# Performance work log

Hardware: AMD Instinct MI355X
Metric: run time of the kernel (lower is better)

The kernel has to match this reference:

```python
import jax, jax.numpy as jnp
import numpy as np

N = 50000        # nodes
E = 800000       # edges
E_PAIR = 200000  # pos/neg link pairs
IN = 256
HID = (512, 256, 160)
NEG_SLOPE = 0.2


def _lin_w(k, i, o):
    s = 1.0 / np.sqrt(i)
    return jax.random.uniform(k, (i, o), jnp.float32, -s, s)


def setup_inputs() -> dict:
    key = jax.random.key(0)
    ks = jax.random.split(key, 16)
    inp = {
        'x': jax.random.normal(ks[0], (N, IN), jnp.float32),
        'w': jax.random.uniform(ks[1], (E,), jnp.float32),
        'src': jax.random.randint(ks[2], (E,), 0, N),
        'dst': jax.random.randint(ks[3], (E,), 0, N),
        'pos_src': jax.random.randint(ks[4], (E_PAIR,), 0, N),
        'pos_dst': jax.random.randint(ks[5], (E_PAIR,), 0, N),
        'neg_src': jax.random.randint(ks[6], (E_PAIR,), 0, N),
        'neg_dst': jax.random.randint(ks[7], (E_PAIR,), 0, N),
        # GraphConv weights/biases
        'W1': _lin_w(ks[8], IN, HID[0]), 'b1': jnp.zeros((HID[0],), jnp.float32),
        'W2': _lin_w(ks[9], HID[0], HID[1]), 'b2': jnp.zeros((HID[1],), jnp.float32),
        'W3': _lin_w(ks[10], HID[1], HID[2]), 'b3': jnp.zeros((HID[2],), jnp.float32),
        # predictor MLP: 160 -> 80 -> 40 -> 1
        'P1': _lin_w(ks[11], HID[2], HID[2] // 2), 'pb1': jnp.zeros((HID[2] // 2,), jnp.float32),
        'P2': _lin_w(ks[12], HID[2] // 2, HID[2] // 4), 'pb2': jnp.zeros((HID[2] // 4,), jnp.float32),
        'P3': _lin_w(ks[13], HID[2] // 4, 1), 'pb3': jnp.zeros((1,), jnp.float32),
    }
    return inp


def _degree_norms(src, dst):
    ones = jnp.ones((E,), jnp.float32)
    out_deg = jnp.clip(jax.ops.segment_sum(ones, src, num_segments=N), 1.0)
    in_deg = jnp.clip(jax.ops.segment_sum(ones, dst, num_segments=N), 1.0)
    # norm='both': D_out^{-1/2} on source side, D_in^{-1/2} on dest side
    return (out_deg ** -0.5)[:, None], (in_deg ** -0.5)[:, None]


def _graph_conv(h, W, b, src, dst, w, out_norm, in_norm, project_first):
    # DGL GraphConv (norm='both', edge_weight=w): scale src feats, multiply
    # messages by edge weight, sum-aggregate, scale by in-degree norm, + bias.
    # DGL projects before aggregation iff in_feats > out_feats (same math).
    h = h * out_norm
    if project_first:
        h = h @ W
    agg = jax.ops.segment_sum(h[src] * w[:, None], dst, num_segments=N)
    if not project_first:
        agg = agg @ W
    return agg * in_norm + b


def _predictor(z, P1, pb1, P2, pb2, P3, pb3):
    z = jax.nn.leaky_relu(z @ P1 + pb1, NEG_SLOPE)
    z = jax.nn.leaky_relu(z @ P2 + pb2, NEG_SLOPE)
    return z @ P3 + pb3


def reference(x, w, src, dst, pos_src, pos_dst, neg_src, neg_dst,
              W1, b1, W2, b2, W3, b3, P1, pb1, P2, pb2, P3, pb3):
    out_norm, in_norm = _degree_norms(src, dst)
    h = _graph_conv(x, W1, b1, src, dst, w, out_norm, in_norm, project_first=False)  # 256<=512
    h = jax.nn.relu(h)
    h = _graph_conv(h, W2, b2, src, dst, w, out_norm, in_norm, project_first=True)   # 512>256
    h = jax.nn.relu(h)
    h = _graph_conv(h, W3, b3, src, dst, w, out_norm, in_norm, project_first=True)   # 256>160
    h_pos = _predictor(h[pos_src] * h[pos_dst], P1, pb1, P2, pb2, P3, pb3)
    h_neg = _predictor(h[neg_src] * h[neg_dst], P1, pb1, P2, pb2, P3, pb3)
    return h_pos, h_neg, h
```

## Files before the change

### kernel.cpp

```cpp
#include <hip/hip_runtime.h>
#include <math.h>

#define NN 50000
#define EE 800000
#define NPAIR 200000

typedef unsigned short u16;
typedef short short8v __attribute__((ext_vector_type(8)));
typedef float float16v __attribute__((ext_vector_type(16)));

__device__ __forceinline__ float leaky(float x){ return x >= 0.f ? x : 0.2f*x; }

__device__ __forceinline__ u16 bfhi(float x){
  union{float f; unsigned u;} v; v.f = x;
  unsigned r = (v.u + 0x7FFFu + ((v.u >> 16) & 1u)) >> 16;
  return (u16)r;
}
__device__ __forceinline__ float bf2f(u16 h){
  union{unsigned u; float f;} v; v.u = ((unsigned)h) << 16; return v.f;
}
__device__ __forceinline__ void split2(float x, float y, unsigned &hp, unsigned &lp){
  u16 hx = bfhi(x), hy = bfhi(y);
  u16 lx = bfhi(x - bf2f(hx)), ly = bfhi(y - bf2f(hy));
  hp = (unsigned)hx | ((unsigned)hy << 16);
  lp = (unsigned)lx | ((unsigned)ly << 16);
}
#define MFMA_BF16 __builtin_amdgcn_mfma_f32_32x32x16_bf16


__global__ void degree_kernel(const int* __restrict__ src, const int* __restrict__ dst,
                              int* cnt_out, int* cnt_in){
  int i = blockIdx.x*blockDim.x + threadIdx.x;
  if(i < EE){
    atomicAdd(&cnt_out[src[i]], 1);
    atomicAdd(&cnt_in[dst[i]], 1);
  }
}

__global__ void norm_kernel(const int* __restrict__ cnt_out, const int* __restrict__ cnt_in,
                            float* __restrict__ out_norm, float* __restrict__ in_norm){
  int i = blockIdx.x*blockDim.x + threadIdx.x;
  if(i < NN){
    int o = cnt_out[i]; if(o < 1) o = 1;
    int d = cnt_in[i];  if(d < 1) d = 1;
    out_norm[i] = 1.f/sqrtf((float)o);
    in_norm[i]  = 1.f/sqrtf((float)d);
  }
}

__global__ void scan_kernel(const int* __restrict__ cnt, int* __restrict__ row_off){
  const int T = 512;
  __shared__ int sums[T];
  int t = threadIdx.x;
  int chunk = (NN + T - 1)/T;
  int base = t*chunk;
  int hi = base + chunk; if(hi > NN) hi = NN;
  int s = 0;
  for(int i = base; i < hi; i++) s += cnt[i];
  sums[t] = s;
  __syncthreads();
  for(int off = 1; off < T; off <<= 1){
    int add = (t >= off) ? sums[t-off] : 0;
    __syncthreads();
    sums[t] += add;
    __syncthreads();
  }
  int run = sums[t] - s;
  for(int i = base; i < hi; i++){ row_off[i] = run; run += cnt[i]; }
  if(t == T-1) row_off[NN] = EE;
}

__global__ void bucket_kernel(const int* __restrict__ src, const int* __restrict__ dst,
                              const float* __restrict__ w, const float* __restrict__ out_norm,
                              const int* __restrict__ row_off,
                              int* fill, int* __restrict__ es, float* __restrict__ ew){
  int i = blockIdx.x*blockDim.x + threadIdx.x;
  if(i < EE){
    int d = dst[i];
    int s = src[i];
    int p = row_off[d] + atomicAdd(&fill[d], 1);
    es[p] = s;
    ew[p] = w[i] * out_norm[s];
  }
}

__global__ void wsplit_kernel(const float* __restrict__ W, int K, int M,
                              u16* __restrict__ Whi, u16* __restrict__ Wlo){
  int i = blockIdx.x*256 + threadIdx.x;
  if(i < K*M){
    int m = i / K, k = i - m*K;
    float a = W[(size_t)k*M + m];
    u16 h = bfhi(a);
    Whi[i] = h;
    Wlo[i] = bfhi(a - bf2f(h));
  }
}

__global__ void psplit_kernel(const float* __restrict__ P1, const float* __restrict__ P2,
                              u16* __restrict__ P1th, u16* __restrict__ P1tl,
                              u16* __restrict__ P2th, u16* __restrict__ P2tl){
  int i = blockIdx.x*256 + threadIdx.x;
  if(i < 96*160){
    int c = i/160, k = i - c*160;
    float v = (c < 80) ? P1[k*80 + c] : 0.f;
    u16 h = bfhi(v);
    P1th[i] = h; P1tl[i] = bfhi(v - bf2f(h));
  }
  if(i < 64*80){
    int c = i/80, k = i - c*80;
    float v = (c < 40) ? P2[k*40 + c] : 0.f;
    u16 h = bfhi(v);
    P2th[i] = h; P2tl[i] = bfhi(v - bf2f(h));
  }
}

template<int F, int MODE>
__global__ __launch_bounds__(256) void agg_kernel(
    const float* __restrict__ feat, const int* __restrict__ es,
    const float* __restrict__ ew, const int* __restrict__ row_off,
    const float* __restrict__ innorm, const float* __restrict__ bias,
    float* __restrict__ out){
  constexpr int F4 = F/4;
  int wid = threadIdx.x >> 6, lane = threadIdx.x & 63;
  int v = blockIdx.x*4 + wid;
  if(v >= NN || lane >= F4) return;
  int s = row_off[v], e = row_off[v+1];
  const float4* f4 = (const float4*)feat;
  float4 a0 = {0,0,0,0}, a1 = {0,0,0,0}, a2 = {0,0,0,0}, a3 = {0,0,0,0};
  int j = s;
  for(; j + 3 < e; j += 4){
    int   i0 = es[j],   i1 = es[j+1], i2 = es[j+2], i3 = es[j+3];
    float w0 = ew[j],   w1 = ew[j+1], w2 = ew[j+2], w3 = ew[j+3];
    float4 r0 = f4[(size_t)i0*F4 + lane];
    float4 r1 = f4[(size_t)i1*F4 + lane];
    float4 r2 = f4[(size_t)i2*F4 + lane];
    float4 r3 = f4[(size_t)i3*F4 + lane];
    a0.x += r0.x*w0; a0.y += r0.y*w0; a0.z += r0.z*w0; a0.w += r0.w*w0;
    a1.x += r1.x*w1; a1.y += r1.y*w1; a1.z += r1.z*w1; a1.w += r1.w*w1;
    a2.x += r2.x*w2; a2.y += r2.y*w2; a2.z += r2.z*w2; a2.w += r2.w*w2;
    a3.x += r3.x*w3; a3.y += r3.y*w3; a3.z += r3.z*w3; a3.w += r3.w*w3;
  }
  for(; j < e; j++){
    int idx = es[j]; float wt = ew[j];
    float4 r = f4[(size_t)idx*F4 + lane];
    a0.x += r.x*wt; a0.y += r.y*wt; a0.z += r.z*wt; a0.w += r.w*wt;
  }
  float4 r;
  r.x = (a0.x+a1.x)+(a2.x+a3.x);
  r.y = (a0.y+a1.y)+(a2.y+a3.y);
  r.z = (a0.z+a1.z)+(a2.z+a3.z);
  r.w = (a0.w+a1.w)+(a2.w+a3.w);
  if(MODE >= 1){
    float inm = innorm[v];
    float4 bb = *(const float4*)&bias[lane*4];
    r.x = r.x*inm + bb.x; r.y = r.y*inm + bb.y;
    r.z = r.z*inm + bb.z; r.w = r.w*inm + bb.w;
    if(MODE == 1){
      r.x = fmaxf(r.x, 0.f); r.y = fmaxf(r.y, 0.f);
      r.z = fmaxf(r.z, 0.f); r.w = fmaxf(r.w, 0.f);
    }
  }
  ((float4*)(out + (size_t)v*F))[lane] = r;
}

template<bool EPI>
__global__ __launch_bounds__(256) void gemm_mfma(
    const float* __restrict__ A, const u16* __restrict__ Bhi, const u16* __restrict__ Blo,
    float* __restrict__ C, int K, int M,
    const float* __restrict__ innorm, const float* __restrict__ bias){
  __shared__ u16 sAhi[128*40];
  __shared__ u16 sAlo[128*40];
  __shared__ u16 sBhi[128*40];
  __shared__ u16 sBlo[128*40];
  int tid = threadIdx.x;
  int row0 = blockIdx.x*128, col0 = blockIdx.y*128;
  int wv = tid >> 6, L = tid & 63;
  int wr = (wv >> 1)*64, wc = (wv & 1)*64;
  int srow = tid >> 1, skh = (tid & 1)*16;

  float16v acc[2][2];
  #pragma unroll
  for(int i = 0; i < 2; i++)
    #pragma unroll
    for(int j = 0; j < 2; j++)
      #pragma unroll
      for(int r = 0; r < 16; r++) acc[i][j][r] = 0.f;

  const float* Arow = A + (size_t)(row0 + srow)*K;
  bool av = (row0 + srow) < NN;
  bool bv = (col0 + srow) < M;
  const u16* bhsrc = Bhi + (size_t)(col0 + srow)*K;
  const u16* blsrc = Blo + (size_t)(col0 + srow)*K;
  const uint4 z4 = make_uint4(0,0,0,0);

  for(int k0 = 0; k0 < K; k0 += 32){
    float4 af0 = {0,0,0,0}, af1 = {0,0,0,0}, af2 = {0,0,0,0}, af3 = {0,0,0,0};
    if(av){
      af0 = *(const float4*)&Arow[k0 + skh];
      af1 = *(const float4*)&Arow[k0 + skh + 4];
      af2 = *(const float4*)&Arow[k0 + skh + 8];
      af3 = *(const float4*)&Arow[k0 + skh + 12];
    }
    uint4 bh0 = z4, bh1 = z4, bl0 = z4, bl1 = z4;
    if(bv){
      bh0 = *(const uint4*)&bhsrc[k0 + skh];
      bh1 = *(const uint4*)&bhsrc[k0 + skh + 8];
      bl0 = *(const uint4*)&blsrc[k0 + skh];
      bl1 = *(const uint4*)&blsrc[k0 + skh + 8];
    }
    unsigned h0,h1,h2,h3,h4,h5,h6,h7, l0,l1,l2,l3,l4,l5,l6,l7;
    split2(af0.x, af0.y, h0, l0); split2(af0.z, af0.w, h1, l1);
    split2(af1.x, af1.y, h2, l2); split2(af1.z, af1.w, h3, l3);
    split2(af2.x, af2.y, h4, l4); split2(af2.z, af2.w, h5, l5);
    split2(af3.x, af3.y, h6, l6); split2(af3.z, af3.w, h7, l7);
    __syncthreads();
    int sa = srow*40 + skh;
    *(uint4*)&sAhi[sa]     = make_uint4(h0,h1,h2,h3);
    *(uint4*)&sAhi[sa + 8] = make_uint4(h4,h5,h6,h7);
    *(uint4*)&sAlo[sa]     = make_uint4(l0,l1,l2,l3);
    *(uint4*)&sAlo[sa + 8] = make_uint4(l4,l5,l6,l7);
    *(uint4*)&sBhi[sa]     = bh0;
    *(uint4*)&sBhi[sa + 8] = bh1;
    *(uint4*)&sBlo[sa]     = bl0;
    *(uint4*)&sBlo[sa + 8] = bl1;
    __syncthreads();
    #pragma unroll
    for(int ks = 0; ks < 2; ks++){
      int ko = ks*16 + (L >> 5)*8;
      int ra0 = (wr + (L & 31))*40 + ko, ra1 = ra0 + 32*40;
      int rb0 = (wc + (L & 31))*40 + ko, rb1 = rb0 + 32*40;
      short8v ah0 = *(const short8v*)&sAhi[ra0];
      short8v ah1 = *(const short8v*)&sAhi[ra1];
      short8v al0 = *(const short8v*)&sAlo[ra0];
      short8v al1 = *(const short8v*)&sAlo[ra1];
      short8v bhf0 = *(const short8v*)&sBhi[rb0];
      short8v bhf1 = *(const short8v*)&sBhi[rb1];
      short8v blf0 = *(const short8v*)&sBlo[rb0];
      short8v blf1 = *(const short8v*)&sBlo[rb1];
      acc[0][0] = MFMA_BF16(ah0, bhf0, acc[0][0], 0,0,0);
      acc[0][0] = MFMA_BF16(al0, bhf0, acc[0][0], 0,0,0);
      acc[0][0] = MFMA_BF16(ah0, blf0, acc[0][0], 0,0,0);
      acc[0][1] = MFMA_BF16(ah0, bhf1, acc[0][1], 0,0,0);
      acc[0][1] = MFMA_BF16(al0, bhf1, acc[0][1], 0,0,0);
      acc[0][1] = MFMA_BF16(ah0, blf1, acc[0][1], 0,0,0);
      acc[1][0] = MFMA_BF16(ah1, bhf0, acc[1][0], 0,0,0);
      acc[1][0] = MFMA_BF16(al1, bhf0, acc[1][0], 0,0,0);
      acc[1][0] = MFMA_BF16(ah1, blf0, acc[1][0], 0,0,0);
      acc[1][1] = MFMA_BF16(ah1, bhf1, acc[1][1], 0,0,0);
      acc[1][1] = MFMA_BF16(al1, bhf1, acc[1][1], 0,0,0);
      acc[1][1] = MFMA_BF16(ah1, blf1, acc[1][1], 0,0,0);
    }
  }

  int cB = L & 31, rq = 4*(L >> 5);
  #pragma unroll
  for(int tr = 0; tr < 2; tr++){
    #pragma unroll
    for(int tc = 0; tc < 2; tc++){
      int c = col0 + wc + tc*32 + cB;
      if(c >= M) continue;
      #pragma unroll
      for(int reg = 0; reg < 16; reg++){
        int r = row0 + wr + tr*32 + (reg & 3) + 8*(reg >> 2) + rq;
        if(r >= NN) continue;
        float v = acc[tr][tc][reg];
        if(EPI) v = fmaxf(v*innorm[r] + bias[c], 0.f);
        C[(size_t)r*M + c] = v;
      }
    }
  }
}

#define ZSTR 168
#define P1STR 24
#define Y1STR 88
__global__ __launch_bounds__(256) void predictor_mfma(
    const float* __restrict__ h3,
    const int* __restrict__ ps, const int* __restrict__ pd,
    const int* __restrict__ ns, const int* __restrict__ nd,
    const u16* __restrict__ P1th, const u16* __restrict__ P1tl,
    const float* __restrict__ pb1,
    const u16* __restrict__ P2th, const u16* __restrict__ P2tl,
    const float* __restrict__ pb2,
    const float* __restrict__ P3, const float* __restrict__ pb3,
    float* __restrict__ out){
  __shared__ u16 smem[26112];
  u16* zh  = smem;
  u16* zl  = smem + 64*ZSTR;
  u16* p1h = smem + 2*64*ZSTR;
  u16* p1l = p1h + 96*P1STR;
  u16* y1h = smem;
  u16* y1l = smem + 64*Y1STR;
  u16* p2h = smem + 2*64*Y1STR;
  u16* p2l = smem + 3*64*Y1STR;
  float* part = (float*)(smem + 4*64*Y1STR);

  int tid = threadIdx.x;
  int pair0 = blockIdx.x*64;
  int w = tid >> 6, L = tid & 63;
  int lrow = L & 31, lk = (L >> 5)*8;

  {
    int p = tid >> 2, sub = tid & 3;
    int q = pair0 + p;
    int a, b;
    if(q < NPAIR){ a = ps[q]; b = pd[q]; }
    else         { a = ns[q-NPAIR]; b = nd[q-NPAIR]; }
    const float4* ra = (const float4*)(h3 + (size_t)a*160);
    const float4* rb = (const float4*)(h3 + (size_t)b*160);
    #pragma unroll
    for(int it = 0; it < 10; it++){
      int g = sub + it*4;
      float4 va = ra[g], vb = rb[g];
      unsigned hp0, lp0, hp1, lp1;
      split2(va.x*vb.x, va.y*vb.y, hp0, lp0);
      split2(va.z*vb.z, va.w*vb.w, hp1, lp1);
      *(uint2*)&zh[p*ZSTR + 4*g] = make_uint2(hp0, hp1);
      *(uint2*)&zl[p*ZSTR + 4*g] = make_uint2(lp0, lp1);
    }
  }

  float16v acc1a, acc1b;
  #pragma unroll
  for(int r = 0; r < 16; r++){ acc1a[r] = 0.f; acc1b[r] = 0.f; }
  int j1 = w, j2 = (w < 2) ? (w + 4) : -1;
  int pt1 = j1/3, ct1 = j1 - pt1*3;
  int pt2 = (j2 >= 0) ? j2/3 : 0;
  int ct2j = (j2 >= 0) ? (j2 - pt2*3) : 0;

  for(int k0 = 0; k0 < 160; k0 += 16){
    __syncthreads();
    if(tid < 192){
      int c = tid >> 1, half = tid & 1;
      uint4 vh = *(const uint4*)&P1th[c*160 + k0 + half*8];
      uint4 vl = *(const uint4*)&P1tl[c*160 + k0 + half*8];
      *(uint4*)&p1h[c*P1STR + half*8] = vh;
      *(uint4*)&p1l[c*P1STR + half*8] = vl;
    }
    __syncthreads();
    {
      short8v ah = *(const short8v*)&zh[(pt1*32 + lrow)*ZSTR + k0 + lk];
      short8v al = *(const short8v*)&zl[(pt1*32 + lrow)*ZSTR + k0 + lk];
      short8v bh = *(const short8v*)&p1h[(ct1*32 + lrow)*P1STR + lk];
      short8v bl = *(const short8v*)&p1l[(ct1*32 + lrow)*P1STR + lk];
      acc1a = MFMA_BF16(ah, bh, acc1a, 0,0,0);
      acc1a = MFMA_BF16(al, bh, acc1a, 0,0,0);
      acc1a = MFMA_BF16(ah, bl, acc1a, 0,0,0);
    }
    if(j2 >= 0){
      short8v ah = *(const short8v*)&zh[(pt2*32 + lrow)*ZSTR + k0 + lk];
      short8v al = *(const short8v*)&zl[(pt2*32 + lrow)*ZSTR + k0 + lk];
      short8v bh = *(const short8v*)&p1h[(ct2j*32 + lrow)*P1STR + lk];
      short8v bl = *(const short8v*)&p1l[(ct2j*32 + lrow)*P1STR + lk];
      acc1b = MFMA_BF16(ah, bh, acc1b, 0,0,0);
      acc1b = MFMA_BF16(al, bh, acc1b, 0,0,0);
      acc1b = MFMA_BF16(ah, bl, acc1b, 0,0,0);
    }
  }
  __syncthreads();

  {
    int c = ct1*32 + lrow;
    if(c < 80){
      float pb = pb1[c];
      #pragma unroll
      for(int r = 0; r < 16; r++){
        int p = pt1*32 + (r & 3) + 8*(r >> 2) + 4*(L >> 5);
        float v = leaky(acc1a[r] + pb);
        u16 h = bfhi(v);
        y1h[p*Y1STR + c] = h;
        y1l[p*Y1STR + c] = bfhi(v - bf2f(h));
      }
    }
  }
  if(j2 >= 0){
    int c = ct2j*32 + lrow;
    if(c < 80){
      float pb = pb1[c];
      #pragma unroll
      for(int r = 0; r < 16; r++){
        int p = pt2*32 + (r & 3) + 8*(r >> 2) + 4*(L >> 5);
        float v = leaky(acc1b[r] + pb);
        u16 h = bfhi(v);
        y1h[p*Y1STR + c] = h;
        y1l[p*Y1STR + c] = bfhi(v - bf2f(h));
      }
    }
  }
  for(int i = tid; i < 640; i += 256){
    int c = i/10, jj = i - c*10;
    *(uint4*)&p2h[c*Y1STR + jj*8] = *(const uint4*)&P2th[c*80 + jj*8];
    *(uint4*)&p2l[c*Y1STR + jj*8] = *(const uint4*)&P2tl[c*80 + jj*8];
  }
  __syncthreads();

  float16v acc2;
  #pragma unroll
  for(int r = 0; r < 16; r++) acc2[r] = 0.f;
  int pt = w & 1, c2t = w >> 1;
  for(int k0 = 0; k0 < 80; k0 += 16){
    short8v ah = *(const short8v*)&y1h[(pt*32 + lrow)*Y1STR + k0 + lk];
    short8v al = *(const short8v*)&y1l[(pt*32 + lrow)*Y1STR + k0 + lk];
    short8v bh = *(const short8v*)&p2h[(c2t*32 + lrow)*Y1STR + k0 + lk];
    short8v bl = *(const short8v*)&p2l[(c2t*32 + lrow)*Y1STR + k0 + lk];
    acc2 = MFMA_BF16(ah, bh, acc2, 0,0,0);
    acc2 = MFMA_BF16(al, bh, acc2, 0,0,0);
    acc2 = MFMA_BF16(ah, bl, acc2, 0,0,0);
  }

  int c2 = c2t*32 + lrow;
  float pb2c = (c2 < 40) ? pb2[c2] : 0.f;
  float p3c  = (c2 < 40) ? P3[c2]  : 0.f;
  float vals[16];
  #pragma unroll
  for(int r = 0; r < 16; r++){
    float v = leaky(acc2[r] + pb2c) * p3c;
    #pragma unroll
    for(int m = 1; m < 32; m <<= 1) v += __shfl_xor(v, m);
    vals[r] = v;
  }
  if(lrow == 0){
    #pragma unroll
    for(int r = 0; r < 16; r++){
      int p = pt*32 + (r & 3) + 8*(r >> 2) + 4*(L >> 5);
      part[c2t*64 + p] = vals[r];
    }
  }
  __syncthreads();
  if(tid < 64) out[pair0 + tid] = (part[tid] + part[64 + tid]) + pb3[0];
}


extern "C" void kernel_launch(void* const* d_in, const int* in_sizes, int n_in,
                              void* d_out, int out_size, void* d_ws, size_t ws_size,
                              hipStream_t stream) {
  const float* x  = (const float*)d_in[0];
  const float* w  = (const float*)d_in[1];
  const int* src  = (const int*)d_in[2];
  const int* dst  = (const int*)d_in[3];
  const int* ps   = (const int*)d_in[4];
  const int* pd   = (const int*)d_in[5];
  const int* ns   = (const int*)d_in[6];
  const int* nd   = (const int*)d_in[7];
  const float* W1 = (const float*)d_in[8];  const float* b1  = (const float*)d_in[9];
  const float* W2 = (const float*)d_in[10]; const float* b2  = (const float*)d_in[11];
  const float* W3 = (const float*)d_in[12]; const float* b3  = (const float*)d_in[13];
  const float* P1 = (const float*)d_in[14]; const float* pb1 = (const float*)d_in[15];
  const float* P2 = (const float*)d_in[16]; const float* pb2 = (const float*)d_in[17];
  const float* P3 = (const float*)d_in[18]; const float* pb3 = (const float*)d_in[19];
  float* out = (float*)d_out;

  char* p = (char*)d_ws;
  auto alloc = [&](size_t bytes)->char*{
    char* r = p; p += (bytes + 255) & ~(size_t)255; return r;
  };
  int*   cnt_out = (int*)  alloc(NN*4);
  int*   cnt_in  = (int*)  alloc(NN*4);
  int*   fill    = (int*)  alloc(NN*4);
  int*   row_off = (int*)  alloc((NN+1)*4);
  float* out_nrm = (float*)alloc(NN*4);
  float* in_nrm  = (float*)alloc(NN*4);
  int*   es      = (int*)  alloc((size_t)EE*4);
  float* ew      = (float*)alloc((size_t)EE*4);
  u16*   w1h     = (u16*)  alloc(256*512*2);
  u16*   w1l     = (u16*)  alloc(256*512*2);
  u16*   w2h     = (u16*)  alloc(512*256*2);
  u16*   w2l     = (u16*)  alloc(512*256*2);
  u16*   w3h     = (u16*)  alloc(256*160*2);
  u16*   w3l     = (u16*)  alloc(256*160*2);
  u16*   p1th    = (u16*)  alloc(96*160*2);
  u16*   p1tl    = (u16*)  alloc(96*160*2);
  u16*   p2th    = (u16*)  alloc(64*80*2);
  u16*   p2tl    = (u16*)  alloc(64*80*2);
  float* bufA    = (float*)alloc((size_t)NN*512*4);
  float* bufB    = (float*)alloc((size_t)NN*256*4);
  float* bufC    = (float*)alloc((size_t)NN*256*4);

  size_t cntPad = (NN*4 + 255) & ~(size_t)255;
  hipMemsetAsync(cnt_out, 0, 3*cntPad, stream);

  degree_kernel<<<(EE+255)/256, 256, 0, stream>>>(src, dst, cnt_out, cnt_in);
  norm_kernel<<<(NN+255)/256, 256, 0, stream>>>(cnt_out, cnt_in, out_nrm, in_nrm);
  scan_kernel<<<1, 512, 0, stream>>>(cnt_in, row_off);
  bucket_kernel<<<(EE+255)/256, 256, 0, stream>>>(src, dst, w, out_nrm, row_off, fill, es, ew);
  wsplit_kernel<<<512, 256, 0, stream>>>(W1, 256, 512, w1h, w1l);
  wsplit_kernel<<<512, 256, 0, stream>>>(W2, 512, 256, w2h, w2l);
  wsplit_kernel<<<160, 256, 0, stream>>>(W3, 256, 160, w3h, w3l);
  psplit_kernel<<<60, 256, 0, stream>>>(P1, P2, p1th, p1tl, p2th, p2tl);

  int aggGrid = (NN + 3)/4;

  agg_kernel<256,0><<<aggGrid, 256, 0, stream>>>(x, es, ew, row_off, nullptr, nullptr, bufC);
  gemm_mfma<true><<<dim3(391,4), 256, 0, stream>>>(bufC, w1h, w1l, bufA, 256, 512, in_nrm, b1);

  gemm_mfma<false><<<dim3(391,2), 256, 0, stream>>>(bufA, w2h, w2l, bufB, 512, 256, nullptr, nullptr);
  agg_kernel<256,1><<<aggGrid, 256, 0, stream>>>(bufB, es, ew, row_off, in_nrm, b2, bufC);

  gemm_mfma<false><<<dim3(391,2), 256, 0, stream>>>(bufC, w3h, w3l, bufB, 256, 160, nullptr, nullptr);
  agg_kernel<160,2><<<aggGrid, 256, 0, stream>>>(bufB, es, ew, row_off, in_nrm, b3, out + 2*NPAIR);

  predictor_mfma<<<(2*NPAIR)/64, 256, 0, stream>>>(out + 2*NPAIR, ps, pd, ns, nd,
                                                   p1th, p1tl, pb1, p2th, p2tl, pb2,
                                                   P3, pb3, out);
}
```

Before: 937.2 us.

## Restructure predictor to per-wave 16-pair tiles with 16x16 MFMA and register A operands

Rewrites the link predictor kernel so each wave owns 16 pairs and builds the Hadamard-product A fragments directly in registers, using 16x16x32 bf16 MFMA instead of 32x32. The LDS staging of z and of P1/P2 tiles is removed, along with the per-k-step block barriers; weights are read straight from global/L1. The goal is less LDS traffic, fewer barriers and less padding waste on the 80- and 40-column outputs. In exchange, weight loads are repeated per wave from cache and the gathers become less coalesced, since each lane reads 8 consecutive floats.

```diff
diff --git a/kernel.cpp b/kernel.cpp
--- a/kernel.cpp
+++ b/kernel.cpp
@@ -8,6 +8,7 @@
 typedef unsigned short u16;
 typedef short short8v __attribute__((ext_vector_type(8)));
 typedef float float16v __attribute__((ext_vector_type(16)));
+typedef float float4v __attribute__((ext_vector_type(4)));
 
 __device__ __forceinline__ float leaky(float x){ return x >= 0.f ? x : 0.2f*x; }
 
@@ -26,6 +27,7 @@
   lp = (unsigned)lx | ((unsigned)ly << 16);
 }
 #define MFMA_BF16 __builtin_amdgcn_mfma_f32_32x32x16_bf16
+#define MFMA16    __builtin_amdgcn_mfma_f32_16x16x32_bf16
 
 
 __global__ void degree_kernel(const int* __restrict__ src, const int* __restrict__ dst,
@@ -271,8 +273,6 @@
   }
 }
 
-#define ZSTR 168
-#define P1STR 24
 #define Y1STR 88
 __global__ __launch_bounds__(256) void predictor_mfma(
     const float* __restrict__ h3,
@@ -284,150 +284,108 @@
     const float* __restrict__ pb2,
     const float* __restrict__ P3, const float* __restrict__ pb3,
     float* __restrict__ out){
-  __shared__ u16 smem[26112];
-  u16* zh  = smem;
-  u16* zl  = smem + 64*ZSTR;
-  u16* p1h = smem + 2*64*ZSTR;
-  u16* p1l = p1h + 96*P1STR;
-  u16* y1h = smem;
-  u16* y1l = smem + 64*Y1STR;
-  u16* p2h = smem + 2*64*Y1STR;
-  u16* p2l = smem + 3*64*Y1STR;
-  float* part = (float*)(smem + 4*64*Y1STR);
+  __shared__ u16 y1h[64*Y1STR];
+  __shared__ u16 y1l[64*Y1STR];
 
   int tid = threadIdx.x;
   int pair0 = blockIdx.x*64;
-  int w = tid >> 6, L = tid & 63;
-  int lrow = L & 31, lk = (L >> 5)*8;
-
-  {
-    int p = tid >> 2, sub = tid & 3;
-    int q = pair0 + p;
-    int a, b;
-    if(q < NPAIR){ a = ps[q]; b = pd[q]; }
-    else         { a = ns[q-NPAIR]; b = nd[q-NPAIR]; }
-    const float4* ra = (const float4*)(h3 + (size_t)a*160);
-    const float4* rb = (const float4*)(h3 + (size_t)b*160);
-    #pragma unroll
-    for(int it = 0; it < 10; it++){
-      int g = sub + it*4;
-      float4 va = ra[g], vb = rb[g];
-      unsigned hp0, lp0, hp1, lp1;
-      split2(va.x*vb.x, va.y*vb.y, hp0, lp0);
-      split2(va.z*vb.z, va.w*vb.w, hp1, lp1);
-      *(uint2*)&zh[p*ZSTR + 4*g] = make_uint2(hp0, hp1);
-      *(uint2*)&zl[p*ZSTR + 4*g] = make_uint2(lp0, lp1);
-    }
-  }
-
-  float16v acc1a, acc1b;
-  #pragma unroll
-  for(int r = 0; r < 16; r++){ acc1a[r] = 0.f; acc1b[r] = 0.f; }
-  int j1 = w, j2 = (w < 2) ? (w + 4) : -1;
-  int pt1 = j1/3, ct1 = j1 - pt1*3;
-  int pt2 = (j2 >= 0) ? j2/3 : 0;
-  int ct2j = (j2 >= 0) ? (j2 - pt2*3) : 0;
-
-  for(int k0 = 0; k0 < 160; k0 += 16){
-    __syncthreads();
-    if(tid < 192){
-      int c = tid >> 1, half = tid & 1;
-      uint4 vh = *(const uint4*)&P1th[c*160 + k0 + half*8];
-      uint4 vl = *(const uint4*)&P1tl[c*160 + k0 + half*8];
-      *(uint4*)&p1h[c*P1STR + half*8] = vh;
-      *(uint4*)&p1l[c*P1STR + half*8] = vl;
-    }
-    __syncthreads();
-    {
-      short8v ah = *(const short8v*)&zh[(pt1*32 + lrow)*ZSTR + k0 + lk];
-      short8v al = *(const short8v*)&zl[(pt1*32 + lrow)*ZSTR + k0 + lk];
-      short8v bh = *(const short8v*)&p1h[(ct1*32 + lrow)*P1STR + lk];
-      short8v bl = *(const short8v*)&p1l[(ct1*32 + lrow)*P1STR + lk];
-      acc1a = MFMA_BF16(ah, bh, acc1a, 0,0,0);
-      acc1a = MFMA_BF16(al, bh, acc1a, 0,0,0);
-      acc1a = MFMA_BF16(ah, bl, acc1a, 0,0,0);
-    }
-    if(j2 >= 0){
-      short8v ah = *(const short8v*)&zh[(pt2*32 + lrow)*ZSTR + k0 + lk];
-      short8v al = *(const short8v*)&zl[(pt2*32 + lrow)*ZSTR + k0 + lk];
-      short8v bh = *(const short8v*)&p1h[(ct2j*32 + lrow)*P1STR + lk];
-      short8v bl = *(const short8v*)&p1l[(ct2j*32 + lrow)*P1STR + lk];
-      acc1b = MFMA_BF16(ah, bh, acc1b, 0,0,0);
-      acc1b = MFMA_BF16(al, bh, acc1b, 0,0,0);
-      acc1b = MFMA_BF16(ah, bl, acc1b, 0,0,0);
+  int w  = tid >> 6;
+  int L  = tid & 63;
+  int lr = L & 15;
+  int lg = L >> 4;
+  int lk = lg*8;
+
+  int q = pair0 + w*16 + lr;
+  int ia, ib;
+  if(q < NPAIR){ ia = ps[q]; ib = pd[q]; }
+  else         { ia = ns[q-NPAIR]; ib = nd[q-NPAIR]; }
+  const float4* ra = (const float4*)(h3 + (size_t)ia*160);
+  const float4* rb = (const float4*)(h3 + (size_t)ib*160);
+
+  float4v acc1[5];
+  #pragma unroll
+  for(int c = 0; c < 5; c++) acc1[c] = (float4v){0.f,0.f,0.f,0.f};
+
+  union U16B { unsigned u[4]; short8v s; };
+
+  #pragma unroll
+  for(int kt = 0; kt < 5; kt++){
+    int k0 = kt*32;
+    int g = (k0 + lk) >> 2;
+    float4 va0 = ra[g], va1 = ra[g+1];
+    float4 vb0 = rb[g], vb1 = rb[g+1];
+    U16B Ah, Al;
+    split2(va0.x*vb0.x, va0.y*vb0.y, Ah.u[0], Al.u[0]);
+    split2(va0.z*vb0.z, va0.w*vb0.w, Ah.u[1], Al.u[1]);
+    split2(va1.x*vb1.x, va1.y*vb1.y, Ah.u[2], Al.u[2]);
+    split2(va1.z*vb1.z, va1.w*vb1.w, Ah.u[3], Al.u[3]);
+    #pragma unroll
+    for(int ct = 0; ct < 5; ct++){
+      int col = ct*16 + lr;
+      short8v bh = *(const short8v*)&P1th[col*160 + k0 + lk];
+      short8v bl = *(const short8v*)&P1tl[col*160 + k0 + lk];
+      acc1[ct] = MFMA16(Ah.s, bh, acc1[ct], 0,0,0);
+      acc1[ct] = MFMA16(Al.s, bh, acc1[ct], 0,0,0);
+      acc1[ct] = MFMA16(Ah.s, bl, acc1[ct], 0,0,0);
+    }
+  }
+
+  #pragma unroll
+  for(int ct = 0; ct < 5; ct++){
+    int c = ct*16 + lr;
+    float pb = pb1[c];
+    #pragma unroll
+    for(int r = 0; r < 4; r++){
+      int p = w*16 + lg*4 + r;
+      float v = leaky(acc1[ct][r] + pb);
+      u16 hh = bfhi(v);
+      y1h[p*Y1STR + c] = hh;
+      y1l[p*Y1STR + c] = bfhi(v - bf2f(hh));
     }
   }
   __syncthreads();
 
-  {
-    int c = ct1*32 + lrow;
-    if(c < 80){
-      float pb = pb1[c];
-      #pragma unroll
-      for(int r = 0; r < 16; r++){
-        int p = pt1*32 + (r & 3) + 8*(r >> 2) + 4*(L >> 5);
-        float v = leaky(acc1a[r] + pb);
-        u16 h = bfhi(v);
-        y1h[p*Y1STR + c] = h;
-        y1l[p*Y1STR + c] = bfhi(v - bf2f(h));
-      }
-    }
-  }
-  if(j2 >= 0){
-    int c = ct2j*32 + lrow;
-    if(c < 80){
-      float pb = pb1[c];
-      #pragma unroll
-      for(int r = 0; r < 16; r++){
-        int p = pt2*32 + (r & 3) + 8*(r >> 2) + 4*(L >> 5);
-        float v = leaky(acc1b[r] + pb);
-        u16 h = bfhi(v);
-        y1h[p*Y1STR + c] = h;
-        y1l[p*Y1STR + c] = bfhi(v - bf2f(h));
-      }
-    }
-  }
-  for(int i = tid; i < 640; i += 256){
-    int c = i/10, jj = i - c*10;
-    *(uint4*)&p2h[c*Y1STR + jj*8] = *(const uint4*)&P2th[c*80 + jj*8];
-    *(uint4*)&p2l[c*Y1STR + jj*8] = *(const uint4*)&P2tl[c*80 + jj*8];
-  }
-  __syncthreads();
-
-  float16v acc2;
-  #pragma unroll
-  for(int r = 0; r < 16; r++) acc2[r] = 0.f;
-  int pt = w & 1, c2t = w >> 1;
-  for(int k0 = 0; k0 < 80; k0 += 16){
-    short8v ah = *(const short8v*)&y1h[(pt*32 + lrow)*Y1STR + k0 + lk];
-    short8v al = *(const short8v*)&y1l[(pt*32 + lrow)*Y1STR + k0 + lk];
-    short8v bh = *(const short8v*)&p2h[(c2t*32 + lrow)*Y1STR + k0 + lk];
-    short8v bl = *(const short8v*)&p2l[(c2t*32 + lrow)*Y1STR + k0 + lk];
-    acc2 = MFMA_BF16(ah, bh, acc2, 0,0,0);
-    acc2 = MFMA_BF16(al, bh, acc2, 0,0,0);
-    acc2 = MFMA_BF16(ah, bl, acc2, 0,0,0);
-  }
-
-  int c2 = c2t*32 + lrow;
-  float pb2c = (c2 < 40) ? pb2[c2] : 0.f;
-  float p3c  = (c2 < 40) ? P3[c2]  : 0.f;
-  float vals[16];
-  #pragma unroll
-  for(int r = 0; r < 16; r++){
-    float v = leaky(acc2[r] + pb2c) * p3c;
-    #pragma unroll
-    for(int m = 1; m < 32; m <<= 1) v += __shfl_xor(v, m);
-    vals[r] = v;
-  }
-  if(lrow == 0){
-    #pragma unroll
-    for(int r = 0; r < 16; r++){
-      int p = pt*32 + (r & 3) + 8*(r >> 2) + 4*(L >> 5);
-      part[c2t*64 + p] = vals[r];
-    }
-  }
-  __syncthreads();
-  if(tid < 64) out[pair0 + tid] = (part[tid] + part[64 + tid]) + pb3[0];
+  float4v acc2[3];
+  #pragma unroll
+  for(int c = 0; c < 3; c++) acc2[c] = (float4v){0.f,0.f,0.f,0.f};
+
+  const short8v z8 = {0,0,0,0,0,0,0,0};
+  #pragma unroll
+  for(int kt = 0; kt < 3; kt++){
+    int k0 = kt*32;
+    bool tail = (kt == 2) && (lg >= 2);
+    int kk = tail ? 64 : (k0 + lk);
+    short8v ah = *(const short8v*)&y1h[(w*16 + lr)*Y1STR + kk];
+    short8v al = *(const short8v*)&y1l[(w*16 + lr)*Y1STR + kk];
+    if(tail){ ah = z8; al = z8; }
+    #pragma unroll
+    for(int ct = 0; ct < 3; ct++){
+      int col = ct*16 + lr;
+      short8v bh = *(const short8v*)&P2th[col*80 + kk];
+      short8v bl = *(const short8v*)&P2tl[col*80 + kk];
+      acc2[ct] = MFMA16(ah, bh, acc2[ct], 0,0,0);
+      acc2[ct] = MFMA16(al, bh, acc2[ct], 0,0,0);
+      acc2[ct] = MFMA16(ah, bl, acc2[ct], 0,0,0);
+    }
+  }
+
+  float pb3v = pb3[0];
+  float pbc0 = 0.f, p3c0 = 0.f, pbc1 = 0.f, p3c1 = 0.f, pbc2 = 0.f, p3c2 = 0.f;
+  { int c0 = lr, c1 = 16 + lr, c2 = 32 + lr;
+    pbc0 = pb2[c0]; p3c0 = P3[c0];
+    pbc1 = pb2[c1]; p3c1 = P3[c1];
+    if(c2 < 40){ pbc2 = pb2[c2]; p3c2 = P3[c2]; } }
+  #pragma unroll
+  for(int r = 0; r < 4; r++){
+    float v = leaky(acc2[0][r] + pbc0) * p3c0
+            + leaky(acc2[1][r] + pbc1) * p3c1
+            + leaky(acc2[2][r] + pbc2) * p3c2;
+    v += __shfl_xor(v, 1);
+    v += __shfl_xor(v, 2);
+    v += __shfl_xor(v, 4);
+    v += __shfl_xor(v, 8);
+    if(lr == 0) out[pair0 + w*16 + lg*4 + r] = v + pb3v;
+  }
 }
 
 
```

Result: slower. 971.8 us (+3.7%).

## Sort link pairs by source node to improve predictor gather locality

Applied to the files above, without the earlier changes.

Adds a counting sort of the positive and negative link pairs by source node: a per-node count, a prefix scan and a bucketing pass build sorted src/dst/original-index arrays. The predictor then reads pairs in sorted order so that rows of h sharing a source node are gathered close together for better cache reuse, and it scatters results back through the saved index. This adds three small kernels plus an indirect output write, and the atomic bucketing makes the order within each bucket nondeterministic. The predictor's h rows total about 32 MB, so the gain from locality may be small.

```diff
diff --git a/kernel.cpp b/kernel.cpp
--- a/kernel.cpp
+++ b/kernel.cpp
@@ -48,7 +48,8 @@
   }
 }
 
-__global__ void scan_kernel(const int* __restrict__ cnt, int* __restrict__ row_off){
+template<int TOTAL>
+__global__ void scan_kernel(const int* __restrict__ cnt, int* __restrict__ off){
   const int T = 512;
   __shared__ int sums[T];
   int t = threadIdx.x;
@@ -59,15 +60,15 @@
   for(int i = base; i < hi; i++) s += cnt[i];
   sums[t] = s;
   __syncthreads();
-  for(int off = 1; off < T; off <<= 1){
-    int add = (t >= off) ? sums[t-off] : 0;
+  for(int o = 1; o < T; o <<= 1){
+    int add = (t >= o) ? sums[t-o] : 0;
     __syncthreads();
     sums[t] += add;
     __syncthreads();
   }
   int run = sums[t] - s;
-  for(int i = base; i < hi; i++){ row_off[i] = run; run += cnt[i]; }
-  if(t == T-1) row_off[NN] = EE;
+  for(int i = base; i < hi; i++){ off[i] = run; run += cnt[i]; }
+  if(t == T-1) off[NN] = TOTAL;
 }
 
 __global__ void bucket_kernel(const int* __restrict__ src, const int* __restrict__ dst,
@@ -81,6 +82,30 @@
     int p = row_off[d] + atomicAdd(&fill[d], 1);
     es[p] = s;
     ew[p] = w[i] * out_norm[s];
+  }
+}
+
+__global__ void pair_count_kernel(const int* __restrict__ ps, const int* __restrict__ ns,
+                                  int* cnt_p){
+  int i = blockIdx.x*256 + threadIdx.x;
+  if(i < 2*NPAIR){
+    int a = (i < NPAIR) ? ps[i] : ns[i-NPAIR];
+    atomicAdd(&cnt_p[a], 1);
+  }
+}
+
+__global__ void pair_bucket_kernel(const int* __restrict__ ps, const int* __restrict__ pd,
+                                   const int* __restrict__ ns, const int* __restrict__ nd,
+                                   const int* __restrict__ poff, int* fill_p,
+                                   int* __restrict__ sa, int* __restrict__ sb,
+                                   int* __restrict__ so_){
+  int i = blockIdx.x*256 + threadIdx.x;
+  if(i < 2*NPAIR){
+    int a, b;
+    if(i < NPAIR){ a = ps[i]; b = pd[i]; }
+    else         { a = ns[i-NPAIR]; b = nd[i-NPAIR]; }
+    int pos = poff[a] + atomicAdd(&fill_p[a], 1);
+    sa[pos] = a; sb[pos] = b; so_[pos] = i;
   }
 }
 
@@ -276,8 +301,8 @@
 #define Y1STR 88
 __global__ __launch_bounds__(256) void predictor_mfma(
     const float* __restrict__ h3,
-    const int* __restrict__ ps, const int* __restrict__ pd,
-    const int* __restrict__ ns, const int* __restrict__ nd,
+    const int* __restrict__ sa, const int* __restrict__ sb,
+    const int* __restrict__ so_,
     const u16* __restrict__ P1th, const u16* __restrict__ P1tl,
     const float* __restrict__ pb1,
     const u16* __restrict__ P2th, const u16* __restrict__ P2tl,
@@ -303,9 +328,7 @@
   {
     int p = tid >> 2, sub = tid & 3;
     int q = pair0 + p;
-    int a, b;
-    if(q < NPAIR){ a = ps[q]; b = pd[q]; }
-    else         { a = ns[q-NPAIR]; b = nd[q-NPAIR]; }
+    int a = sa[q], b = sb[q];
     const float4* ra = (const float4*)(h3 + (size_t)a*160);
     const float4* rb = (const float4*)(h3 + (size_t)b*160);
     #pragma unroll
@@ -427,7 +450,7 @@
     }
   }
   __syncthreads();
-  if(tid < 64) out[pair0 + tid] = (part[tid] + part[64 + tid]) + pb3[0];
+  if(tid < 64) out[so_[pair0 + tid]] = (part[tid] + part[64 + tid]) + pb3[0];
 }
 
 
@@ -457,11 +480,17 @@
   int*   cnt_out = (int*)  alloc(NN*4);
   int*   cnt_in  = (int*)  alloc(NN*4);
   int*   fill    = (int*)  alloc(NN*4);
+  int*   cnt_p   = (int*)  alloc(NN*4);
+  int*   fill_p  = (int*)  alloc(NN*4);
   int*   row_off = (int*)  alloc((NN+1)*4);
+  int*   poff    = (int*)  alloc((NN+1)*4);
   float* out_nrm = (float*)alloc(NN*4);
   float* in_nrm  = (float*)alloc(NN*4);
   int*   es      = (int*)  alloc((size_t)EE*4);
   float* ew      = (float*)alloc((size_t)EE*4);
+  int*   sa      = (int*)  alloc((size_t)2*NPAIR*4);
+  int*   sb      = (int*)  alloc((size_t)2*NPAIR*4);
+  int*   so_     = (int*)  alloc((size_t)2*NPAIR*4);
   u16*   w1h     = (u16*)  alloc(256*512*2);
   u16*   w1l     = (u16*)  alloc(256*512*2);
   u16*   w2h     = (u16*)  alloc(512*256*2);
@@ -477,12 +506,18 @@
   float* bufC    = (float*)alloc((size_t)NN*256*4);
 
   size_t cntPad = (NN*4 + 255) & ~(size_t)255;
-  hipMemsetAsync(cnt_out, 0, 3*cntPad, stream);
+  hipMemsetAsync(cnt_out, 0, 5*cntPad, stream);
 
   degree_kernel<<<(EE+255)/256, 256, 0, stream>>>(src, dst, cnt_out, cnt_in);
   norm_kernel<<<(NN+255)/256, 256, 0, stream>>>(cnt_out, cnt_in, out_nrm, in_nrm);
-  scan_kernel<<<1, 512, 0, stream>>>(cnt_in, row_off);
+  scan_kernel<EE><<<1, 512, 0, stream>>>(cnt_in, row_off);
   bucket_kernel<<<(EE+255)/256, 256, 0, stream>>>(src, dst, w, out_nrm, row_off, fill, es, ew);
+
+  pair_count_kernel<<<(2*NPAIR+255)/256, 256, 0, stream>>>(ps, ns, cnt_p);
+  scan_kernel<2*NPAIR><<<1, 512, 0, stream>>>(cnt_p, poff);
+  pair_bucket_kernel<<<(2*NPAIR+255)/256, 256, 0, stream>>>(ps, pd, ns, nd, poff, fill_p,
+                                                            sa, sb, so_);
+
   wsplit_kernel<<<512, 256, 0, stream>>>(W1, 256, 512, w1h, w1l);
   wsplit_kernel<<<512, 256, 0, stream>>>(W2, 512, 256, w2h, w2l);
   wsplit_kernel<<<160, 256, 0, stream>>>(W3, 256, 160, w3h, w3l);
@@ -499,7 +534,7 @@
   gemm_mfma<false><<<dim3(391,2), 256, 0, stream>>>(bufC, w3h, w3l, bufB, 256, 160, nullptr, nullptr);
   agg_kernel<160,2><<<aggGrid, 256, 0, stream>>>(bufB, es, ew, row_off, in_nrm, b3, out + 2*NPAIR);
 
-  predictor_mfma<<<(2*NPAIR)/64, 256, 0, stream>>>(out + 2*NPAIR, ps, pd, ns, nd,
+  predictor_mfma<<<(2*NPAIR)/64, 256, 0, stream>>>(out + 2*NPAIR, sa, sb, so_,
                                                    p1th, p1tl, pb1, p2th, p2tl, pb2,
                                                    P3, pb3, out);
 }
```

Result: slower. 1.061 ms (+13.2%).
